# Optimization experiments

Hardware: AMD Instinct MI355X
Metric: run time of the kernel (lower is better)

The kernel has to match this reference:

```python
import jax, jax.numpy as jnp
import numpy as np

C = 256          # in_channels == out_channels
L = 131072       # sequence length (multiple of BL)
BL = 64          # dilation == sliding-attention block length
CQ = C // 2      # q/k channels (r1=2)
CV = C // 2      # v channels (r2=2)
ALPHA = 1.0
EPS_IN = 1e-5    # InstanceNorm eps


def setup_inputs() -> dict:
    key = jax.random.key(0)
    ks = jax.random.split(key, 16)
    s = 0.05
    return {
        "x": jax.random.normal(ks[0], (1, C, L), jnp.float32),
        "f": jax.random.normal(ks[1], (1, C, L), jnp.float32),
        "mask": jnp.ones((1, 1, L), jnp.float32),
        # ConvFeedForward: Conv1d(C, C, 3, padding=BL, dilation=BL)
        "Wff": jax.random.normal(ks[2], (C, C, 3), jnp.float32) * s,
        "bff": jax.random.normal(ks[3], (C,), jnp.float32) * s,
        # AttLayer 1x1 convs
        "Wq": jax.random.normal(ks[4], (CQ, C), jnp.float32) * s,
        "bq": jax.random.normal(ks[5], (CQ,), jnp.float32) * s,
        "Wk": jax.random.normal(ks[6], (CQ, C), jnp.float32) * s,
        "bk": jax.random.normal(ks[7], (CQ,), jnp.float32) * s,
        "Wv": jax.random.normal(ks[8], (CV, C), jnp.float32) * s,
        "bv": jax.random.normal(ks[9], (CV,), jnp.float32) * s,
        "Wo": jax.random.normal(ks[10], (C, CV), jnp.float32) * s,
        "bo": jax.random.normal(ks[11], (C,), jnp.float32) * s,
        # AttModule.conv_1x1
        "Wc": jax.random.normal(ks[12], (C, C), jnp.float32) * s,
        "bc": jax.random.normal(ks[13], (C,), jnp.float32) * s,
    }


def _conv1x1(W, b, x):  # x: (B, Cin, L)
    return jnp.einsum('oc,bcl->bol', W, x) + b[None, :, None]


def _forward(x, f, mask, Wff, bff, Wq, bq, Wk, bk, Wv, bv, Wo, bo, Wc, bc):
    # --- ConvFeedForward: dilated conv + ReLU (same-length output) ---
    out = jax.lax.conv_general_dilated(
        x, Wff, window_strides=(1,), padding=[(BL, BL)], rhs_dilation=(BL,),
        dimension_numbers=('NCH', 'OIH', 'NCH')) + bff[None, :, None]
    out = jax.nn.relu(out)  # (1, C, L)

    # --- InstanceNorm1d (affine=False, biased var) ---
    mu = out.mean(axis=-1, keepdims=True)
    var = out.var(axis=-1, keepdims=True)
    xn = (out - mu) * jax.lax.rsqrt(var + EPS_IN)

    # --- AttLayer (sliding_att, decoder: value from f) ---
    q = _conv1x1(Wq, bq, xn)   # (1, CQ, L)
    k = _conv1x1(Wk, bk, xn)   # (1, CQ, L)
    v = _conv1x1(Wv, bv, f)    # (1, CV, L)

    nb = L // BL
    half = BL // 2
    pm = mask[:, 0:1, :]                         # (1,1,L) padding mask
    # pad halo of BL//2 zeros on each side of k, v, padding_mask
    kp = jnp.pad(k, ((0, 0), (0, 0), (half, half)))
    vp = jnp.pad(v, ((0, 0), (0, 0), (half, half)))
    mp = jnp.pad(pm, ((0, 0), (0, 0), (half, half)))
    # window index: block i sees [i*BL, i*BL + 2*BL) of the padded sequence
    idx = jnp.arange(nb)[:, None] * BL + jnp.arange(2 * BL)[None, :]  # (nb, 2BL)
    kw = kp[:, :, idx]   # (1, CQ, nb, 2BL)
    vw = vp[:, :, idx]   # (1, CV, nb, 2BL)
    mw = mp[:, 0, idx]   # (1, nb, 2BL)

    # window mask: query i attends keys [i, i+BL) within the 2BL window
    d = jnp.arange(2 * BL)[None, :] - jnp.arange(BL)[:, None]
    wm = ((d >= 0) & (d < BL)).astype(x.dtype)          # (BL, 2BL)
    fm = wm[None, None] * mw[:, :, None, :]             # (1, nb, BL, 2BL)

    qb = q.reshape(1, CQ, nb, BL)
    energy = jnp.einsum('bcnl,bcnm->bnlm', qb, kw) / np.sqrt(CQ).astype(x.dtype)
    att = jax.nn.softmax(energy + jnp.log(fm + 1e-6), axis=-1) * fm
    ov = jnp.einsum('bcnm,bnlm->bcnl', vw, att)         # (1, CV, nb, BL)
    oo = jnp.einsum('oc,bcnl->bonl', Wo, jax.nn.relu(ov)) + bo[None, :, None, None]
    att_out = oo.reshape(1, C, L) * pm                  # (1, C, L)

    # --- scaled residual + 1x1 conv + (dropout=identity) + masked residual ---
    h = ALPHA * att_out + out
    h = _conv1x1(Wc, bc, h)
    return (x + h) * mask


def reference(x, f, mask, Wff, bff, Wq, bq, Wk, bk, Wv, bv, Wo, bo, Wc, bc):
    return _forward(x, f, mask, Wff, bff, Wq, bq, Wk, bk, Wv, bv, Wo, bo, Wc, bc)
```

## Files before the change

kernel.cpp:

```cpp
#include <hip/hip_runtime.h>

#define L_LEN 131072
#define NB    2048
#define NT    1024

typedef unsigned short u16;
typedef __attribute__((ext_vector_type(4))) float f32x4;
typedef __attribute__((ext_vector_type(8))) short s16x8;
typedef __attribute__((ext_vector_type(4))) short s16x4;

#define WS_OUTT  0ull
#define WS_QT    67108864ull
#define WS_PSUM  100663296ull
#define WS_PSQ   101711872ull
#define WS_MEAN  102760448ull
#define WS_RSTD  102761472ull
#define WS_WFFB  102762496ull
#define WS_WQKB  103155712ull
#define WS_WVB   103286784ull
#define WS_WOB   103352320ull
#define WS_WCB   103417856ull
#define WS_BQKP  103548928ull
#define WS_ZP    103549952ull

__device__ __forceinline__ u16 f2bf(float v){
  union { float f; unsigned u; } a; a.f = v;
  unsigned r = a.u + 0x7fffu + ((a.u >> 16) & 1u);
  return (u16)(r >> 16);
}
__device__ __forceinline__ float bf2f(u16 u){
  union { unsigned u; float f; } a; a.u = ((unsigned)u) << 16; return a.f;
}
__device__ __forceinline__ unsigned cvtpk(float a, float b){
  unsigned r;
  asm("v_cvt_pk_bf16_f32 %0, %1, %2" : "=v"(r) : "v"(a), "v"(b));
  return r;
}
__device__ __forceinline__ f32x4 mfma16(s16x8 a, s16x8 b, f32x4 c){
  return __builtin_amdgcn_mfma_f32_16x16x32_bf16(a, b, c, 0, 0, 0);
}
__device__ __forceinline__ s16x8 ld8(const void* p){ return *(const s16x8*)p; }
__device__ __forceinline__ void gl_lds16(const void* g, void* l){
  __builtin_amdgcn_global_load_lds(
      (const __attribute__((address_space(1))) unsigned int*)g,
      (__attribute__((address_space(3))) unsigned int*)l, 16, 0, 0);
}

__global__ __launch_bounds__(256) void k_prep(
    const float* __restrict__ Wff, const float* __restrict__ Wv,
    const float* __restrict__ Wo,  const float* __restrict__ Wc,
    short* __restrict__ wffb, short* __restrict__ wvb,
    short* __restrict__ wob,  short* __restrict__ wcb, u16* __restrict__ zp)
{
  int i = blockIdx.x * 256 + threadIdx.x;
  if (i < 196608){
    int o = i / 768, kk = i % 768;
    int t = kk >> 8, c = kk & 255;
    wffb[i] = (short)f2bf(Wff[(o*256 + c)*3 + t]);
  } else if (i < 229376){ int j = i - 196608; wvb[j] = (short)f2bf(Wv[j]); }
  else if (i < 262144){ int j = i - 229376; wob[j] = (short)f2bf(Wo[j]); }
  else if (i < 327680){ int j = i - 262144; wcb[j] = (short)f2bf(Wc[j]); }
  if (blockIdx.x == 0 && threadIdx.x < 32) zp[threadIdx.x] = 0;
}

__global__ __launch_bounds__(256) void k_xbfT(
    const float* __restrict__ x, u16* __restrict__ xbfT)
{
  __shared__ u16 t[64*264];
  const int l0 = blockIdx.x * 64, tid = threadIdx.x;
  const int chb = tid >> 4, pq = tid & 15;
  #pragma unroll
  for (int rep = 0; rep < 16; ++rep){
    const int ch = rep*16 + chb;
    const int pos0 = pq*4;
    f32x4 v = *(const f32x4*)(x + (size_t)ch*L_LEN + l0 + pos0);
    const unsigned u01 = cvtpk(v[0], v[1]), u23 = cvtpk(v[2], v[3]);
    t[(pos0+0)*264 + ch] = (u16)(u01 & 0xffffu);
    t[(pos0+1)*264 + ch] = (u16)(u01 >> 16);
    t[(pos0+2)*264 + ch] = (u16)(u23 & 0xffffu);
    t[(pos0+3)*264 + ch] = (u16)(u23 >> 16);
  }
  __syncthreads();
  #pragma unroll
  for (int rep = 0; rep < 8; ++rep){
    const int idx = rep*256 + tid;
    const int row = idx >> 5, j = idx & 31;
    s16x8 vv = ld8(&t[row*264 + 8*j]);
    *(s16x8*)(xbfT + (size_t)(l0 + row)*256 + 8*j) = vv;
  }
}

__global__ __launch_bounds__(256, 4) void k_conv(
    const u16* __restrict__ xbfT, const short* __restrict__ wffb,
    const float* __restrict__ bff, const u16* __restrict__ zp,
    u16* __restrict__ outT, float* __restrict__ psum, float* __restrict__ psq)
{
  __shared__ u16 sm[16384];
  const int bid = blockIdx.x;
  const int swz = (bid & 7) * 256 + (bid >> 3);
  const int oh = swz & 1, pt = swz >> 1;
  const int l0 = pt * 128;
  const int tid = threadIdx.x;
  const int w = tid >> 6, lane = tid & 63, p = lane & 15, g = lane >> 4;
  const int wm = w >> 1, wn = w & 1;

  auto fsw = [](int r){ return ((r >> 2) ^ r) & 3; };

  auto stage = [&](int ks, int buf){
    const int t = ks >> 3, c0 = (ks & 7) * 32;
    #pragma unroll
    for (int gi = 0; gi < 2; ++gi){
      const int r = 32*w + 16*gi + (lane >> 2);
      const int slot = lane & 3;
      const int cb = (slot ^ fsw(r)) * 8;
      {
        const short* srcA = wffb + (size_t)(128*oh + r)*768 + t*256 + c0 + cb;
        gl_lds16(srcA, &sm[buf*8192 + (32*w + 16*gi)*32]);
      }
      {
        const int wpos = l0 + 64*t - 64 + r;
        const u16* srcB = (wpos >= 0 && wpos < L_LEN)
                        ? (xbfT + (size_t)wpos*256 + c0 + cb)
                        : (zp + (lane & 3)*8);
        gl_lds16(srcB, &sm[buf*8192 + 4096 + (32*w + 16*gi)*32]);
      }
    }
  };

  stage(0, 0);
  __syncthreads();

  f32x4 acc[4][4] = {};
  #pragma unroll 1
  for (int ks = 0; ks < 24; ++ks){
    const int cur = ks & 1;
    if (ks < 23) stage(ks + 1, cur ^ 1);
    s16x8 a[4], b[4];
    #pragma unroll
    for (int fm = 0; fm < 4; ++fm){
      const int r = 64*wm + 16*fm + p;
      a[fm] = ld8(&sm[cur*8192 + r*32 + ((g ^ fsw(r)) * 8)]);
    }
    #pragma unroll
    for (int fn = 0; fn < 4; ++fn){
      const int r = 64*wn + 16*fn + p;
      b[fn] = ld8(&sm[cur*8192 + 4096 + r*32 + ((g ^ fsw(r)) * 8)]);
    }
    #pragma unroll
    for (int fm = 0; fm < 4; ++fm){
      #pragma unroll
      for (int fn = 0; fn < 4; ++fn)
        acc[fm][fn] = mfma16(a[fm], b[fn], acc[fm][fn]);
    }
    __syncthreads();
  }

  float* sf = (float*)sm;
  #pragma unroll
  for (int fm = 0; fm < 4; ++fm){
    const int ol = 64*wm + 16*fm + 4*g;
    float sv[4] = {0,0,0,0}, qv[4] = {0,0,0,0};
    #pragma unroll
    for (int fn = 0; fn < 4; ++fn){
      const int pos = l0 + 64*wn + 16*fn + p;
      s16x4 pk;
      #pragma unroll
      for (int i = 0; i < 4; ++i){
        float val = fmaxf(acc[fm][fn][i] + bff[128*oh + ol + i], 0.f);
        pk[i] = (short)f2bf(val);
        sv[i] += val; qv[i] += val*val;
      }
      *(s16x4*)(outT + (size_t)pos*256 + 128*oh + ol) = pk;
    }
    #pragma unroll
    for (int i = 0; i < 4; ++i){
      #pragma unroll
      for (int d = 1; d < 16; d <<= 1){
        sv[i] += __shfl_xor(sv[i], d, 16);
        qv[i] += __shfl_xor(qv[i], d, 16);
      }
    }
    if (p == 0){
      #pragma unroll
      for (int i = 0; i < 4; ++i){
        sf[(wn*128 + ol + i)*2 + 0] = sv[i];
        sf[(wn*128 + ol + i)*2 + 1] = qv[i];
      }
    }
  }
  __syncthreads();
  if (tid < 128){
    psum[(size_t)(128*oh + tid)*NT + pt] = sf[(0 + tid)*2 + 0] + sf[(128 + tid)*2 + 0];
    psq [(size_t)(128*oh + tid)*NT + pt] = sf[(0 + tid)*2 + 1] + sf[(128 + tid)*2 + 1];
  }
}

__global__ __launch_bounds__(256) void k_stats(
    const float* __restrict__ psum, const float* __restrict__ psq,
    float* __restrict__ mean, float* __restrict__ rstd)
{
  __shared__ float ss[256], sq[256];
  const int ch = blockIdx.x, tid = threadIdx.x;
  float a = 0.f, b = 0.f;
  for (int j = tid; j < NT; j += 256){ a += psum[(size_t)ch*NT + j]; b += psq[(size_t)ch*NT + j]; }
  ss[tid] = a; sq[tid] = b;
  __syncthreads();
  for (int st = 128; st > 0; st >>= 1){
    if (tid < st){ ss[tid] += ss[tid+st]; sq[tid] += sq[tid+st]; }
    __syncthreads();
  }
  if (tid == 0){
    float m = ss[0] / (float)L_LEN;
    float v = sq[0] / (float)L_LEN - m*m;
    mean[ch] = m;
    rstd[ch] = rsqrtf(v + 1e-5f);
  }
}

__global__ __launch_bounds__(256) void k_adj(
    const float* __restrict__ Wq, const float* __restrict__ Wk,
    const float* __restrict__ bq, const float* __restrict__ bk,
    const float* __restrict__ mean, const float* __restrict__ rstd,
    short* __restrict__ wqkb, float* __restrict__ bqkp)
{
  __shared__ float red[256];
  const int o = blockIdx.x, c = threadIdx.x;
  const float* src = (o < 128) ? (Wq + (size_t)o*256) : (Wk + (size_t)(o-128)*256);
  const float bias = (o < 128) ? bq[o] : bk[o-128];
  float wv = src[c] * rstd[c];
  wqkb[o*256 + c] = (short)f2bf(wv);
  red[c] = wv * mean[c];
  __syncthreads();
  for (int st = 128; st > 0; st >>= 1){
    if (c < st) red[c] += red[c+st];
    __syncthreads();
  }
  if (c == 0) bqkp[o] = bias - red[0];
}

__global__ __launch_bounds__(512, 4) void k_v(
    const float* __restrict__ fin, const short* __restrict__ wvb,
    const float* __restrict__ bv, u16* __restrict__ vout)
{
  __shared__ u16 xs[2*128*40];
  const int wg = blockIdx.x, l0 = wg * 128;
  const int tid = threadIdx.x;
  const int w = tid >> 6, lane = tid & 63, p = lane & 15, g = lane >> 4;
  const int cl = tid >> 4, posq = tid & 15;

  {
    #pragma unroll
    for (int u = 0; u < 2; ++u){
      const int row = 8*posq + 4*u;
      f32x4 v = *(const f32x4*)(fin + (size_t)cl*L_LEN + l0 + row);
      const unsigned r01 = cvtpk(v[0], v[1]);
      const unsigned r23 = cvtpk(v[2], v[3]);
      xs[(row+0)*40 + (cl ^ (8*(((row+0)>>2)&3)))] = (u16)(r01 & 0xffffu);
      xs[(row+1)*40 + (cl ^ (8*(((row+1)>>2)&3)))] = (u16)(r01 >> 16);
      xs[(row+2)*40 + (cl ^ (8*(((row+2)>>2)&3)))] = (u16)(r23 & 0xffffu);
      xs[(row+3)*40 + (cl ^ (8*(((row+3)>>2)&3)))] = (u16)(r23 >> 16);
    }
  }
  __syncthreads();

  f32x4 acc[8] = {};
  #pragma unroll 1
  for (int cg = 0; cg < 8; ++cg){
    const int cur = (cg & 1) * 5120;
    const int nxt = ((cg + 1) & 1) * 5120;
    f32x4 vv[2];
    const bool have = (cg < 7);
    if (have){
      #pragma unroll
      for (int u = 0; u < 2; ++u){
        const int row = 8*posq + 4*u;
        vv[u] = *(const f32x4*)(fin + (size_t)((cg+1)*32 + cl)*L_LEN + l0 + row);
      }
    }
    s16x8 af = ld8(wvb + (size_t)(16*w + p)*256 + cg*32 + 8*g);
    #pragma unroll
    for (int fn = 0; fn < 8; ++fn){
      const int row = 16*fn + p;
      s16x8 b = ld8(&xs[cur + row*40 + ((8*g) ^ (8*((row>>2)&3)))]);
      acc[fn] = mfma16(af, b, acc[fn]);
    }
    if (have){
      #pragma unroll
      for (int u = 0; u < 2; ++u){
        const int row = 8*posq + 4*u;
        const unsigned r01 = cvtpk(vv[u][0], vv[u][1]);
        const unsigned r23 = cvtpk(vv[u][2], vv[u][3]);
        xs[nxt + (row+0)*40 + (cl ^ (8*(((row+0)>>2)&3)))] = (u16)(r01 & 0xffffu);
        xs[nxt + (row+1)*40 + (cl ^ (8*(((row+1)>>2)&3)))] = (u16)(r01 >> 16);
        xs[nxt + (row+2)*40 + (cl ^ (8*(((row+2)>>2)&3)))] = (u16)(r23 & 0xffffu);
        xs[nxt + (row+3)*40 + (cl ^ (8*(((row+3)>>2)&3)))] = (u16)(r23 >> 16);
      }
    }
    __syncthreads();
  }
  #pragma unroll
  for (int fn = 0; fn < 8; ++fn){
    #pragma unroll
    for (int i = 0; i < 4; ++i){
      const int cv = 16*w + 4*g + i;
      vout[(size_t)cv*L_LEN + l0 + 16*fn + p] = f2bf(acc[fn][i] + bv[cv]);
    }
  }
}

__global__ __launch_bounds__(512, 2) void k_qk(
    const u16* __restrict__ outT, const short* __restrict__ wqkb,
    const float* __restrict__ bqkp, u16* __restrict__ qT, u16* __restrict__ kT)
{
  extern __shared__ u16 tile[];
  const int wg = blockIdx.x, l0 = wg * 128;
  const int tid = threadIdx.x;
  const int w = tid >> 6, lane = tid & 63, p = lane & 15, g = lane >> 4;
  #pragma unroll
  for (int rep = 0; rep < 8; ++rep){
    const int idx = rep*512 + tid;
    const int r = idx >> 5, cc = idx & 31;
    s16x8 vput = ld8(outT + (size_t)(l0 + r)*256 + cc*8);
    *(s16x8*)(&tile[r*256 + ((cc*8) ^ ((r&7)<<3))]) = vput;
  }
  __syncthreads();
  f32x4 acc[2][8] = {};
  #pragma unroll
  for (int kk = 0; kk < 8; ++kk){
    s16x8 af[2];
    af[0] = ld8(wqkb + (size_t)(32*w +      p)*256 + 32*kk + 8*g);
    af[1] = ld8(wqkb + (size_t)(32*w + 16 + p)*256 + 32*kk + 8*g);
    #pragma unroll
    for (int fn = 0; fn < 8; ++fn){
      const int r = 16*fn + p;
      s16x8 b = ld8(&tile[r*256 + ((32*kk + 8*g) ^ ((r&7)<<3))]);
      acc[0][fn] = mfma16(af[0], b, acc[0][fn]);
      acc[1][fn] = mfma16(af[1], b, acc[1][fn]);
    }
  }
  #pragma unroll
  for (int fm = 0; fm < 2; ++fm){
    const int R0 = 32*w + 16*fm + 4*g;
    #pragma unroll
    for (int fn = 0; fn < 8; ++fn){
      s16x4 pk;
      #pragma unroll
      for (int i = 0; i < 4; ++i) pk[i] = (short)f2bf(acc[fm][fn][i] + bqkp[R0+i]);
      const size_t row = (size_t)(l0 + 16*fn + p);
      if (R0 < 128) *(s16x4*)(qT + row*128 + R0)       = pk;
      else          *(s16x4*)(kT + row*128 + R0 - 128) = pk;
    }
  }
}

__global__ __launch_bounds__(256, 4) void k_attn(
    const u16* __restrict__ qT, const u16* __restrict__ kT,
    const u16* __restrict__ vg, const short* __restrict__ wob,
    const float* __restrict__ bo, const float* __restrict__ mask,
    u16* __restrict__ outT)
{
  __shared__ u16 klds[16384];
  __shared__ float maskw[128];
  const int tid = threadIdx.x;
  const int w = tid >> 6, lane = tid & 63, p = lane & 15, g = lane >> 4;
  const int n = blockIdx.x, s = n * 64;
  const float SCALE = 0.08838834764831845f;

  #pragma unroll
  for (int rep = 0; rep < 8; ++rep){
    const int idx = rep*256 + tid;
    const int m = idx >> 4, cc = idx & 15;
    const int gpos = s - 32 + m;
    s16x8 vput = {};
    if (gpos >= 0 && gpos < L_LEN) vput = ld8(kT + (size_t)gpos*128 + cc*8);
    *(s16x8*)(&klds[m*128 + ((cc*8) ^ ((m&7)<<3))]) = vput;
  }
  if (tid < 128){
    const int gp = s - 32 + tid;
    maskw[tid] = (gp >= 0 && gp < L_LEN) ? mask[gp] : 0.f;
  }
  __syncthreads();

  f32x4 e[8] = {};
  #pragma unroll
  for (int kk = 0; kk < 4; ++kk){
    s16x8 aq = ld8(qT + (size_t)(s + 16*w + p)*128 + 32*kk + 8*g);
    #pragma unroll
    for (int fn = 0; fn < 8; ++fn){
      const int m = 16*fn + p;
      s16x8 b = ld8(&klds[m*128 + ((32*kk + 8*g) ^ ((m&7)<<3))]);
      e[fn] = mfma16(aq, b, e[fn]);
    }
  }
  float M[4] = {-1e30f,-1e30f,-1e30f,-1e30f};
  float S[4] = {0.f,0.f,0.f,0.f};
  #pragma unroll
  for (int fn = 0; fn < 8; ++fn){
    #pragma unroll
    for (int i = 0; i < 4; ++i){
      const int mm = 16*fn + p;
      const int l_ = 16*w + 4*g + i;
      const int d = mm - l_;
      const float fmv = (d >= 0 && d < 64) ? maskw[mm] : 0.f;
      const float z = e[fn][i]*SCALE + __logf(fmv + 1e-6f);
      e[fn][i] = z;
      M[i] = fmaxf(M[i], z);
    }
  }
  #pragma unroll
  for (int i = 0; i < 4; ++i){
    #pragma unroll
    for (int d = 1; d < 16; d <<= 1) M[i] = fmaxf(M[i], __shfl_xor(M[i], d, 16));
  }
  #pragma unroll
  for (int fn = 0; fn < 8; ++fn){
    #pragma unroll
    for (int i = 0; i < 4; ++i){
      const float pv = __expf(e[fn][i] - M[i]);
      e[fn][i] = pv;
      S[i] += pv;
    }
  }
  #pragma unroll
  for (int i = 0; i < 4; ++i){
    #pragma unroll
    for (int d = 1; d < 16; d <<= 1) S[i] += __shfl_xor(S[i], d, 16);
  }
  float rinv[4];
  #pragma unroll
  for (int i = 0; i < 4; ++i) rinv[i] = 1.f / S[i];
  __syncthreads();
  #pragma unroll
  for (int fn = 0; fn < 8; ++fn){
    #pragma unroll
    for (int i = 0; i < 4; ++i){
      const int mm = 16*fn + p;
      const int l_ = 16*w + 4*g + i;
      const int d = mm - l_;
      const float fmv = (d >= 0 && d < 64) ? maskw[mm] : 0.f;
      klds[l_*128 + (mm ^ ((l_&7)<<3))] = f2bf(e[fn][i] * rinv[i] * fmv);
    }
  }
  __syncthreads();

  f32x4 accp[2][4] = {};
  #pragma unroll
  for (int kk = 0; kk < 4; ++kk){
    int gp0 = s - 32 + 32*kk + 8*g;
    gp0 = max(0, min(gp0, L_LEN - 8));
    s16x8 a0 = ld8(vg + (size_t)(32*w +      p)*L_LEN + gp0);
    s16x8 a1 = ld8(vg + (size_t)(32*w + 16 + p)*L_LEN + gp0);
    #pragma unroll
    for (int fn = 0; fn < 4; ++fn){
      const int l_ = 16*fn + p;
      s16x8 b = ld8(&klds[l_*128 + ((32*kk + 8*g) ^ ((l_&7)<<3))]);
      accp[0][fn] = mfma16(a0, b, accp[0][fn]);
      accp[1][fn] = mfma16(a1, b, accp[1][fn]);
    }
  }
  #pragma unroll
  for (int fm = 0; fm < 2; ++fm){
    #pragma unroll
    for (int fn = 0; fn < 4; ++fn){
      const int l_ = 16*fn + p;
      s16x4 pk;
      #pragma unroll
      for (int i = 0; i < 4; ++i) pk[i] = (short)f2bf(fmaxf(accp[fm][fn][i], 0.f));
      const int cv0 = 32*w + 16*fm + 4*g;
      *(s16x4*)(&klds[8192 + l_*128 + (cv0 ^ ((l_&7)<<3))]) = pk;
    }
  }
  __syncthreads();

  f32x4 acco[4][4] = {};
  #pragma unroll
  for (int kk = 0; kk < 4; ++kk){
    s16x8 a[4];
    #pragma unroll
    for (int fm = 0; fm < 4; ++fm)
      a[fm] = ld8(wob + (size_t)(64*w + 16*fm + p)*128 + 32*kk + 8*g);
    #pragma unroll
    for (int fn = 0; fn < 4; ++fn){
      const int l_ = 16*fn + p;
      s16x8 b = ld8(&klds[8192 + l_*128 + ((32*kk + 8*g) ^ ((l_&7)<<3))]);
      #pragma unroll
      for (int fm = 0; fm < 4; ++fm) acco[fm][fn] = mfma16(a[fm], b, acco[fm][fn]);
    }
  }
  #pragma unroll
  for (int fm = 0; fm < 4; ++fm){
    const int o0 = 64*w + 16*fm + 4*g;
    #pragma unroll
    for (int fn = 0; fn < 4; ++fn){
      const int l_ = 16*fn + p;
      const float pml = maskw[32 + l_];
      u16* hp = outT + (size_t)(s + l_)*256 + o0;
      s16x4 res = *(const s16x4*)hp;
      s16x4 pk;
      #pragma unroll
      for (int i = 0; i < 4; ++i){
        float hv = (acco[fm][fn][i] + bo[o0+i]) * pml + bf2f((u16)res[i]);
        pk[i] = (short)f2bf(hv);
      }
      *(s16x4*)hp = pk;
    }
  }
}

__global__ __launch_bounds__(512, 2) void k_wc(
    const u16* __restrict__ hT, const short* __restrict__ wcb,
    const float* __restrict__ bc, const float* __restrict__ x,
    const float* __restrict__ mask, float* __restrict__ dout)
{
  extern __shared__ u16 tile[];
  const int wg = blockIdx.x, l0 = wg * 128;
  const int tid = threadIdx.x;
  const int w = tid >> 6, lane = tid & 63, p = lane & 15, g = lane >> 4;
  #pragma unroll
  for (int rep = 0; rep < 8; ++rep){
    const int idx = rep*512 + tid;
    const int r = idx >> 5, cc = idx & 31;
    s16x8 vput = ld8(hT + (size_t)(l0 + r)*256 + cc*8);
    *(s16x8*)(&tile[r*256 + ((cc*8) ^ ((r&7)<<3))]) = vput;
  }
  __syncthreads();
  f32x4 acc[2][8] = {};
  #pragma unroll
  for (int kk = 0; kk < 8; ++kk){
    s16x8 af[2];
    af[0] = ld8(wcb + (size_t)(32*w +      p)*256 + 32*kk + 8*g);
    af[1] = ld8(wcb + (size_t)(32*w + 16 + p)*256 + 32*kk + 8*g);
    #pragma unroll
    for (int fn = 0; fn < 8; ++fn){
      const int r = 16*fn + p;
      s16x8 b = ld8(&tile[r*256 + ((32*kk + 8*g) ^ ((r&7)<<3))]);
      acc[0][fn] = mfma16(af[0], b, acc[0][fn]);
      acc[1][fn] = mfma16(af[1], b, acc[1][fn]);
    }
  }
  #pragma unroll
  for (int fm = 0; fm < 2; ++fm){
    const int o0 = 32*w + 16*fm + 4*g;
    #pragma unroll
    for (int fn = 0; fn < 8; ++fn){
      const int pos = l0 + 16*fn + p;
      const float mk = mask[pos];
      #pragma unroll
      for (int i = 0; i < 4; ++i){
        const size_t idx = (size_t)(o0+i)*L_LEN + pos;
        dout[idx] = (x[idx] + acc[fm][fn][i] + bc[o0+i]) * mk;
      }
    }
  }
}

extern "C" void kernel_launch(void* const* d_in, const int* in_sizes, int n_in,
                              void* d_out, int out_size, void* d_ws, size_t ws_size,
                              hipStream_t stream)
{
  (void)in_sizes; (void)n_in; (void)out_size; (void)ws_size;
  const float* x    = (const float*)d_in[0];
  const float* f    = (const float*)d_in[1];
  const float* mask = (const float*)d_in[2];
  const float* Wff  = (const float*)d_in[3];
  const float* bff  = (const float*)d_in[4];
  const float* Wq   = (const float*)d_in[5];
  const float* bq   = (const float*)d_in[6];
  const float* Wk   = (const float*)d_in[7];
  const float* bk   = (const float*)d_in[8];
  const float* Wv   = (const float*)d_in[9];
  const float* bv   = (const float*)d_in[10];
  const float* Wo   = (const float*)d_in[11];
  const float* bo   = (const float*)d_in[12];
  const float* Wc   = (const float*)d_in[13];
  const float* bc   = (const float*)d_in[14];

  char* ws = (char*)d_ws;
  u16*   outT = (u16*)(ws + WS_OUTT);
  u16*   qT   = (u16*)(ws + WS_QT);
  float* psum = (float*)(ws + WS_PSUM);
  float* psq  = (float*)(ws + WS_PSQ);
  float* mean = (float*)(ws + WS_MEAN);
  float* rstd = (float*)(ws + WS_RSTD);
  short* wffb = (short*)(ws + WS_WFFB);
  short* wqkb = (short*)(ws + WS_WQKB);
  short* wvb  = (short*)(ws + WS_WVB);
  short* wob  = (short*)(ws + WS_WOB);
  short* wcb  = (short*)(ws + WS_WCB);
  float* bqkp = (float*)(ws + WS_BQKP);
  u16*   zp   = (u16*)(ws + WS_ZP);

  u16* vbuf = (u16*)d_out;
  u16* ktb  = (u16*)((char*)d_out + 33554432);
  u16* xbfT = (u16*)((char*)d_out + 67108864);

  (void)hipFuncSetAttribute((const void*)k_qk,
                            hipFuncAttributeMaxDynamicSharedMemorySize, 65536);
  (void)hipFuncSetAttribute((const void*)k_wc,
                            hipFuncAttributeMaxDynamicSharedMemorySize, 65536);

  k_prep <<<1280, 256, 0, stream>>>(Wff, Wv, Wo, Wc, wffb, wvb, wob, wcb, zp);
  k_xbfT <<<2048, 256, 0, stream>>>(x, xbfT);
  k_conv <<<2048, 256, 0, stream>>>(xbfT, wffb, bff, zp, outT, psum, psq);
  k_stats<<<256,  256, 0, stream>>>(psum, psq, mean, rstd);
  k_adj  <<<256,  256, 0, stream>>>(Wq, Wk, bq, bk, mean, rstd, wqkb, bqkp);
  k_v    <<<NT,   512, 0, stream>>>(f, wvb, bv, vbuf);
  k_qk   <<<NT,   512, 65536, stream>>>(outT, wqkb, bqkp, qT, ktb);
  k_attn <<<NB,   256, 0, stream>>>(qT, ktb, vbuf, wob, bo, mask, outT);
  k_wc   <<<NT,   512, 65536, stream>>>(outT, wcb, bc, x, mask, (float*)d_out);
}
```

Before: 376.8 us.

## Retile qk and wc GEMMs into 128x128 tiles with double-buffered direct-to-LDS staging

The qk and wc 1x1-conv GEMMs are reorganised from 512-thread blocks that each stage a full 128x256 activation tile into 64KB LDS into 256-thread blocks. Each block computes a 128x128 output half and streams 32-wide K slices of both the weight and activation operands through a double-buffered 32KB LDS buffer using global-to-LDS loads. Block IDs are swizzled so that the two output halves of the same position tile run on different slots. The aim is to overlap loads with MFMA work, raise occupancy and reuse A fragments from LDS. The cost is that activation tiles are read twice, once per output half, and there is a barrier on every K step.

```diff
diff --git a/kernel.cpp b/kernel.cpp
--- a/kernel.cpp
+++ b/kernel.cpp
@@ -308,47 +308,74 @@
   }
 }
 
-__global__ __launch_bounds__(512, 2) void k_qk(
+__global__ __launch_bounds__(256, 4) void k_qk(
     const u16* __restrict__ outT, const short* __restrict__ wqkb,
     const float* __restrict__ bqkp, u16* __restrict__ qT, u16* __restrict__ kT)
 {
-  extern __shared__ u16 tile[];
-  const int wg = blockIdx.x, l0 = wg * 128;
+  __shared__ u16 sm[16384];
+  const int bid = blockIdx.x;
+  const int swz = (bid & 7) * 256 + (bid >> 3);
+  const int oh = swz & 1, pt = swz >> 1;
+  const int l0 = pt * 128;
   const int tid = threadIdx.x;
   const int w = tid >> 6, lane = tid & 63, p = lane & 15, g = lane >> 4;
-  #pragma unroll
-  for (int rep = 0; rep < 8; ++rep){
-    const int idx = rep*512 + tid;
-    const int r = idx >> 5, cc = idx & 31;
-    s16x8 vput = ld8(outT + (size_t)(l0 + r)*256 + cc*8);
-    *(s16x8*)(&tile[r*256 + ((cc*8) ^ ((r&7)<<3))]) = vput;
-  }
-  __syncthreads();
-  f32x4 acc[2][8] = {};
-  #pragma unroll
-  for (int kk = 0; kk < 8; ++kk){
-    s16x8 af[2];
-    af[0] = ld8(wqkb + (size_t)(32*w +      p)*256 + 32*kk + 8*g);
-    af[1] = ld8(wqkb + (size_t)(32*w + 16 + p)*256 + 32*kk + 8*g);
-    #pragma unroll
-    for (int fn = 0; fn < 8; ++fn){
-      const int r = 16*fn + p;
-      s16x8 b = ld8(&tile[r*256 + ((32*kk + 8*g) ^ ((r&7)<<3))]);
-      acc[0][fn] = mfma16(af[0], b, acc[0][fn]);
-      acc[1][fn] = mfma16(af[1], b, acc[1][fn]);
-    }
-  }
-  #pragma unroll
-  for (int fm = 0; fm < 2; ++fm){
-    const int R0 = 32*w + 16*fm + 4*g;
-    #pragma unroll
-    for (int fn = 0; fn < 8; ++fn){
+  const int wm = w >> 1, wn = w & 1;
+
+  auto fsw = [](int r){ return ((r >> 2) ^ r) & 3; };
+
+  auto stage = [&](int ks, int buf){
+    const int c0 = ks * 32;
+    #pragma unroll
+    for (int gi = 0; gi < 2; ++gi){
+      const int r = 32*w + 16*gi + (lane >> 2);
+      const int cb = ((lane & 3) ^ fsw(r)) * 8;
+      const short* srcA = wqkb + (size_t)(128*oh + r)*256 + c0 + cb;
+      gl_lds16(srcA, &sm[buf*8192 + (32*w + 16*gi)*32]);
+      const u16* srcB = outT + (size_t)(l0 + r)*256 + c0 + cb;
+      gl_lds16(srcB, &sm[buf*8192 + 4096 + (32*w + 16*gi)*32]);
+    }
+  };
+
+  stage(0, 0);
+  __syncthreads();
+
+  f32x4 acc[4][4] = {};
+  #pragma unroll 1
+  for (int ks = 0; ks < 8; ++ks){
+    const int cur = ks & 1;
+    if (ks < 7) stage(ks + 1, cur ^ 1);
+    s16x8 a[4], b[4];
+    #pragma unroll
+    for (int fm = 0; fm < 4; ++fm){
+      const int r = 64*wm + 16*fm + p;
+      a[fm] = ld8(&sm[cur*8192 + r*32 + ((g ^ fsw(r)) * 8)]);
+    }
+    #pragma unroll
+    for (int fn = 0; fn < 4; ++fn){
+      const int r = 64*wn + 16*fn + p;
+      b[fn] = ld8(&sm[cur*8192 + 4096 + r*32 + ((g ^ fsw(r)) * 8)]);
+    }
+    #pragma unroll
+    for (int fm = 0; fm < 4; ++fm){
+      #pragma unroll
+      for (int fn = 0; fn < 4; ++fn)
+        acc[fm][fn] = mfma16(a[fm], b[fn], acc[fm][fn]);
+    }
+    __syncthreads();
+  }
+
+  u16* dst = (oh == 0) ? qT : kT;
+  #pragma unroll
+  for (int fm = 0; fm < 4; ++fm){
+    const int R0 = 64*wm + 16*fm + 4*g;
+    #pragma unroll
+    for (int fn = 0; fn < 4; ++fn){
+      const int pos = l0 + 64*wn + 16*fn + p;
       s16x4 pk;
       #pragma unroll
-      for (int i = 0; i < 4; ++i) pk[i] = (short)f2bf(acc[fm][fn][i] + bqkp[R0+i]);
-      const size_t row = (size_t)(l0 + 16*fn + p);
-      if (R0 < 128) *(s16x4*)(qT + row*128 + R0)       = pk;
-      else          *(s16x4*)(kT + row*128 + R0 - 128) = pk;
+      for (int i = 0; i < 4; ++i)
+        pk[i] = (short)f2bf(acc[fm][fn][i] + bqkp[128*oh + R0 + i]);
+      *(s16x4*)(dst + (size_t)pos*128 + R0) = pk;
     }
   }
 }
@@ -507,48 +534,75 @@
   }
 }
 
-__global__ __launch_bounds__(512, 2) void k_wc(
+__global__ __launch_bounds__(256, 4) void k_wc(
     const u16* __restrict__ hT, const short* __restrict__ wcb,
     const float* __restrict__ bc, const float* __restrict__ x,
     const float* __restrict__ mask, float* __restrict__ dout)
 {
-  extern __shared__ u16 tile[];
-  const int wg = blockIdx.x, l0 = wg * 128;
+  __shared__ u16 sm[16384];
+  const int bid = blockIdx.x;
+  const int swz = (bid & 7) * 256 + (bid >> 3);
+  const int oh = swz & 1, pt = swz >> 1;
+  const int l0 = pt * 128;
   const int tid = threadIdx.x;
   const int w = tid >> 6, lane = tid & 63, p = lane & 15, g = lane >> 4;
-  #pragma unroll
-  for (int rep = 0; rep < 8; ++rep){
-    const int idx = rep*512 + tid;
-    const int r = idx >> 5, cc = idx & 31;
-    s16x8 vput = ld8(hT + (size_t)(l0 + r)*256 + cc*8);
-    *(s16x8*)(&tile[r*256 + ((cc*8) ^ ((r&7)<<3))]) = vput;
-  }
-  __syncthreads();
-  f32x4 acc[2][8] = {};
-  #pragma unroll
-  for (int kk = 0; kk < 8; ++kk){
-    s16x8 af[2];
-    af[0] = ld8(wcb + (size_t)(32*w +      p)*256 + 32*kk + 8*g);
-    af[1] = ld8(wcb + (size_t)(32*w + 16 + p)*256 + 32*kk + 8*g);
-    #pragma unroll
-    for (int fn = 0; fn < 8; ++fn){
-      const int r = 16*fn + p;
-      s16x8 b = ld8(&tile[r*256 + ((32*kk + 8*g) ^ ((r&7)<<3))]);
-      acc[0][fn] = mfma16(af[0], b, acc[0][fn]);
-      acc[1][fn] = mfma16(af[1], b, acc[1][fn]);
-    }
-  }
-  #pragma unroll
-  for (int fm = 0; fm < 2; ++fm){
-    const int o0 = 32*w + 16*fm + 4*g;
-    #pragma unroll
-    for (int fn = 0; fn < 8; ++fn){
-      const int pos = l0 + 16*fn + p;
+  const int wm = w >> 1, wn = w & 1;
+
+  auto fsw = [](int r){ return ((r >> 2) ^ r) & 3; };
+
+  auto stage = [&](int ks, int buf){
+    const int c0 = ks * 32;
+    #pragma unroll
+    for (int gi = 0; gi < 2; ++gi){
+      const int r = 32*w + 16*gi + (lane >> 2);
+      const int cb = ((lane & 3) ^ fsw(r)) * 8;
+      const short* srcA = wcb + (size_t)(128*oh + r)*256 + c0 + cb;
+      gl_lds16(srcA, &sm[buf*8192 + (32*w + 16*gi)*32]);
+      const u16* srcB = hT + (size_t)(l0 + r)*256 + c0 + cb;
+      gl_lds16(srcB, &sm[buf*8192 + 4096 + (32*w + 16*gi)*32]);
+    }
+  };
+
+  stage(0, 0);
+  __syncthreads();
+
+  f32x4 acc[4][4] = {};
+  #pragma unroll 1
+  for (int ks = 0; ks < 8; ++ks){
+    const int cur = ks & 1;
+    if (ks < 7) stage(ks + 1, cur ^ 1);
+    s16x8 a[4], b[4];
+    #pragma unroll
+    for (int fm = 0; fm < 4; ++fm){
+      const int r = 64*wm + 16*fm + p;
+      a[fm] = ld8(&sm[cur*8192 + r*32 + ((g ^ fsw(r)) * 8)]);
+    }
+    #pragma unroll
+    for (int fn = 0; fn < 4; ++fn){
+      const int r = 64*wn + 16*fn + p;
+      b[fn] = ld8(&sm[cur*8192 + 4096 + r*32 + ((g ^ fsw(r)) * 8)]);
+    }
+    #pragma unroll
+    for (int fm = 0; fm < 4; ++fm){
+      #pragma unroll
+      for (int fn = 0; fn < 4; ++fn)
+        acc[fm][fn] = mfma16(a[fm], b[fn], acc[fm][fn]);
+    }
+    __syncthreads();
+  }
+
+  #pragma unroll
+  for (int fm = 0; fm < 4; ++fm){
+    const int ol = 64*wm + 16*fm + 4*g;
+    #pragma unroll
+    for (int fn = 0; fn < 4; ++fn){
+      const int pos = l0 + 64*wn + 16*fn + p;
       const float mk = mask[pos];
       #pragma unroll
       for (int i = 0; i < 4; ++i){
-        const size_t idx = (size_t)(o0+i)*L_LEN + pos;
-        dout[idx] = (x[idx] + acc[fm][fn][i] + bc[o0+i]) * mk;
+        const int o = 128*oh + ol + i;
+        const size_t idx = (size_t)o*L_LEN + pos;
+        dout[idx] = (x[idx] + acc[fm][fn][i] + bc[o]) * mk;
       }
     }
   }
@@ -594,18 +648,13 @@
   u16* ktb  = (u16*)((char*)d_out + 33554432);
   u16* xbfT = (u16*)((char*)d_out + 67108864);
 
-  (void)hipFuncSetAttribute((const void*)k_qk,
-                            hipFuncAttributeMaxDynamicSharedMemorySize, 65536);
-  (void)hipFuncSetAttribute((const void*)k_wc,
-                            hipFuncAttributeMaxDynamicSharedMemorySize, 65536);
-
   k_prep <<<1280, 256, 0, stream>>>(Wff, Wv, Wo, Wc, wffb, wvb, wob, wcb, zp);
   k_xbfT <<<2048, 256, 0, stream>>>(x, xbfT);
   k_conv <<<2048, 256, 0, stream>>>(xbfT, wffb, bff, zp, outT, psum, psq);
   k_stats<<<256,  256, 0, stream>>>(psum, psq, mean, rstd);
   k_adj  <<<256,  256, 0, stream>>>(Wq, Wk, bq, bk, mean, rstd, wqkb, bqkp);
   k_v    <<<NT,   512, 0, stream>>>(f, wvb, bv, vbuf);
-  k_qk   <<<NT,   512, 65536, stream>>>(outT, wqkb, bqkp, qT, ktb);
+  k_qk   <<<2048, 256, 0, stream>>>(outT, wqkb, bqkp, qT, ktb);
   k_attn <<<NB,   256, 0, stream>>>(qT, ktb, vbuf, wob, bo, mask, outT);
-  k_wc   <<<NT,   512, 65536, stream>>>(outT, wcb, bc, x, mask, (float*)d_out);
-}
+  k_wc   <<<2048, 256, 0, stream>>>(outT, wcb, bc, x, mask, (float*)d_out);
+}
```

After: 386.8 us. 1.03x slower.
